# Performance work log

Hardware: AMD Instinct MI355X
Metric: run time of the kernel (lower is better)

## Reference

```python
import jax, jax.numpy as jnp
import numpy as np

EPSILON_BASE = 0.1
N_ITERS = 10


def setup_inputs() -> dict:
    key = jax.random.key(0)
    k1, k2 = jax.random.split(key)
    N, D = 8192, 512
    embeddings = jax.random.normal(k1, (N, D), dtype=jnp.float32)
    target_noise = jax.random.normal(k2, (N, D), dtype=jnp.float32)
    return {"embeddings": embeddings, "target_noise": target_noise}


def _l2_normalize(x, axis=1, eps=1e-12):
    # matches torch.nn.functional.normalize (divide by max(norm, eps))
    norm = jnp.sqrt(jnp.sum(x * x, axis=axis, keepdims=True))
    return x / jnp.maximum(norm, eps)


def _sinkhorn(x, y):
    n, d = x.shape
    # normalize_embeddings=True path
    x = _l2_normalize(x, axis=1)
    y = _l2_normalize(y, axis=1)
    epsilon = EPSILON_BASE * 2.0
    # squared euclidean cost: C[i,j] = ||x_i - y_j||^2  (cdist p=2, squared)
    sq_x = jnp.sum(x * x, axis=1, keepdims=True)          # (n,1)
    sq_y = jnp.sum(y * y, axis=1, keepdims=True)          # (n,1)
    C = jnp.maximum(sq_x + sq_y.T - 2.0 * (x @ y.T), 0.0)  # (n,n)
    log_K = -C / epsilon

    def body(carry, _):
        log_u, log_v = carry
        log_u = -jax.nn.logsumexp(log_K + log_v[None, :], axis=1)
        log_v = -jax.nn.logsumexp(log_K.T + log_u[None, :], axis=1)
        return (log_u, log_v), None

    init = (jnp.zeros(n, dtype=x.dtype), jnp.zeros(n, dtype=y.dtype))
    (log_u, log_v), _ = jax.lax.scan(body, init, None, length=N_ITERS)

    log_P = log_u[:, None] + log_K + log_v[None, :]
    P = jnp.clip(jnp.exp(log_P), 0.0, 1.0)
    distance = jnp.sum(P * C) / n

    # nan/inf fallback: 1 - mean cosine similarity (x, y already unit norm)
    fallback = 1.0 - jnp.mean(jnp.sum(x * y, axis=1))
    bad = jnp.isnan(distance) | jnp.isinf(distance)
    return jnp.where(bad, fallback, distance)


def reference(embeddings, target_noise):
    if embeddings.ndim == 3:
        embeddings = embeddings.reshape(-1, embeddings.shape[-1])
        target_noise = target_noise.reshape(-1, target_noise.shape[-1])
    return _sinkhorn(embeddings, target_noise)
```

## Files before the change

kernel.cpp:

```cpp
#include <hip/hip_runtime.h>
#include <hip/hip_bf16.h>
#include <hip/hip_fp16.h>
#include <stdint.h>

#define NROW 8192
#define DIM  512
#define LN2   0.6931471805599453f
#define TEN_LOG2E 14.426950408889634f

typedef __attribute__((ext_vector_type(8))) short short8;
typedef __attribute__((ext_vector_type(4))) float f32x4;
typedef __attribute__((ext_vector_type(2))) float f32x2;

__device__ __forceinline__ float block_sum256(float v) {
  #pragma unroll
  for (int off = 32; off > 0; off >>= 1) v += __shfl_down(v, off, 64);
  __shared__ float sb[4];
  const int w = threadIdx.x >> 6;
  if ((threadIdx.x & 63) == 0) sb[w] = v;
  __syncthreads();
  return sb[0] + sb[1] + sb[2] + sb[3];
}

__global__ __launch_bounds__(256) void init_kernel(float* __restrict__ colrcp,
                                                   float* __restrict__ diagacc,
                                                   float* __restrict__ distacc) {
  const int g = blockIdx.x * 256 + threadIdx.x;
  colrcp[g] = 1.0f;
  if (g == 0) { diagacc[0] = 0.f; distacc[0] = 0.f; }
}

__global__ __launch_bounds__(256) void normalize_kernel(
    const float* __restrict__ X, const float* __restrict__ Y,
    __hip_bfloat16* __restrict__ Xn, __hip_bfloat16* __restrict__ Yn,
    float* __restrict__ diagacc) {
  const int wave = threadIdx.x >> 6, lane = threadIdx.x & 63;
  float dsum = 0.f;
  #pragma unroll
  for (int rr = 0; rr < 4; rr++) {
    const int row = blockIdx.x * 16 + wave * 4 + rr;
    const float4* xr = (const float4*)(X + (size_t)row * DIM);
    const float4* yr = (const float4*)(Y + (size_t)row * DIM);
    float4 x0 = xr[lane], x1 = xr[lane + 64];
    float4 y0 = yr[lane], y1 = yr[lane + 64];
    float sx = x0.x*x0.x + x0.y*x0.y + x0.z*x0.z + x0.w*x0.w
             + x1.x*x1.x + x1.y*x1.y + x1.z*x1.z + x1.w*x1.w;
    float sy = y0.x*y0.x + y0.y*y0.y + y0.z*y0.z + y0.w*y0.w
             + y1.x*y1.x + y1.y*y1.y + y1.z*y1.z + y1.w*y1.w;
    float sxy = x0.x*y0.x + x0.y*y0.y + x0.z*y0.z + x0.w*y0.w
              + x1.x*y1.x + x1.y*y1.y + x1.z*y1.z + x1.w*y1.w;
    #pragma unroll
    for (int off = 1; off < 64; off <<= 1) {
      sx  += __shfl_xor(sx, off, 64);
      sy  += __shfl_xor(sy, off, 64);
      sxy += __shfl_xor(sxy, off, 64);
    }
    const float rx = 1.0f / fmaxf(sqrtf(sx), 1e-12f);
    const float ry = 1.0f / fmaxf(sqrtf(sy), 1e-12f);
    if (lane == 0) dsum += sxy * rx * ry;
    ushort4 px, py;
    { __hip_bfloat16 b;
      b = __float2bfloat16(x0.x*rx); px.x = *(unsigned short*)&b;
      b = __float2bfloat16(x0.y*rx); px.y = *(unsigned short*)&b;
      b = __float2bfloat16(x0.z*rx); px.z = *(unsigned short*)&b;
      b = __float2bfloat16(x0.w*rx); px.w = *(unsigned short*)&b;
      b = __float2bfloat16(y0.x*ry); py.x = *(unsigned short*)&b;
      b = __float2bfloat16(y0.y*ry); py.y = *(unsigned short*)&b;
      b = __float2bfloat16(y0.z*ry); py.z = *(unsigned short*)&b;
      b = __float2bfloat16(y0.w*ry); py.w = *(unsigned short*)&b;
    }
    ((ushort4*)(Xn + (size_t)row * DIM))[lane] = px;
    ((ushort4*)(Yn + (size_t)row * DIM))[lane] = py;
    { __hip_bfloat16 b;
      b = __float2bfloat16(x1.x*rx); px.x = *(unsigned short*)&b;
      b = __float2bfloat16(x1.y*rx); px.y = *(unsigned short*)&b;
      b = __float2bfloat16(x1.z*rx); px.z = *(unsigned short*)&b;
      b = __float2bfloat16(x1.w*rx); px.w = *(unsigned short*)&b;
      b = __float2bfloat16(y1.x*ry); py.x = *(unsigned short*)&b;
      b = __float2bfloat16(y1.y*ry); py.y = *(unsigned short*)&b;
      b = __float2bfloat16(y1.z*ry); py.z = *(unsigned short*)&b;
      b = __float2bfloat16(y1.w*ry); py.w = *(unsigned short*)&b;
    }
    ((ushort4*)(Xn + (size_t)row * DIM))[lane + 64] = px;
    ((ushort4*)(Yn + (size_t)row * DIM))[lane + 64] = py;
  }
  if (lane == 0) atomicAdd(diagacc, dsum);
}

__global__ __launch_bounds__(256) void gemm_kernel(
    const __hip_bfloat16* __restrict__ A, const __hip_bfloat16* __restrict__ B,
    uint8_t* __restrict__ K, uint8_t* __restrict__ KT) {
  __shared__ short As[128 * 32];
  __shared__ short Bs[128 * 32];
  const int m0 = blockIdx.y * 128;
  const int n0 = blockIdx.x * 128;
  const int t = threadIdx.x;
  const int wave = t >> 6, lane = t & 63;
  const int wm = (wave & 1) * 64, wn = (wave >> 1) * 64;
  const int fr = lane & 15;
  const int fq = lane >> 4;

  f32x4 acc[4][4];
  #pragma unroll
  for (int i = 0; i < 4; i++)
    #pragma unroll
    for (int j = 0; j < 4; j++) acc[i][j] = (f32x4)0.f;

  const int L0 = t, L1 = t + 256;
  const int ar0 = L0 >> 2, ac0 = L0 & 3;
  const int ar1 = L1 >> 2, ac1 = L1 & 3;
  const int4* Ag = (const int4*)A;
  const int4* Bg = (const int4*)B;

  for (int kt = 0; kt < 16; ++kt) {
    const int kb = kt * 4;
    int4 a0 = Ag[(size_t)(m0 + ar0) * 64 + kb + ac0];
    int4 a1 = Ag[(size_t)(m0 + ar1) * 64 + kb + ac1];
    int4 b0 = Bg[(size_t)(n0 + ar0) * 64 + kb + ac0];
    int4 b1 = Bg[(size_t)(n0 + ar1) * 64 + kb + ac1];
    __syncthreads();
    ((int4*)As)[L0] = a0;
    ((int4*)As)[L1] = a1;
    ((int4*)Bs)[L0] = b0;
    ((int4*)Bs)[L1] = b1;
    __syncthreads();
    short8 af[4], bfr[4];
    #pragma unroll
    for (int i = 0; i < 4; i++) {
      af[i]  = *(const short8*)&As[(wm + i * 16 + fr) * 32 + fq * 8];
      bfr[i] = *(const short8*)&Bs[(wn + i * 16 + fr) * 32 + fq * 8];
    }
    #pragma unroll
    for (int i = 0; i < 4; i++)
      #pragma unroll
      for (int j = 0; j < 4; j++)
        acc[i][j] = __builtin_amdgcn_mfma_f32_16x16x32_bf16(af[i], bfr[j], acc[i][j], 0, 0, 0);
  }
  #pragma unroll
  for (int i = 0; i < 4; i++) {
    #pragma unroll
    for (int j = 0; j < 4; j++) {
      const int R  = wm + i * 16 + fq * 4;
      const int Cc = wn + j * 16 + fr;
      float v0 = exp2f(fminf(acc[i][j][0], 1.0f) * TEN_LOG2E);
      float v1 = exp2f(fminf(acc[i][j][1], 1.0f) * TEN_LOG2E);
      float v2 = exp2f(fminf(acc[i][j][2], 1.0f) * TEN_LOG2E);
      float v3 = exp2f(fminf(acc[i][j][3], 1.0f) * TEN_LOG2E);
      int pk = 0;
      pk = __builtin_amdgcn_cvt_pk_fp8_f32(v0, v1, pk, false);
      pk = __builtin_amdgcn_cvt_pk_fp8_f32(v2, v3, pk, true);
      *(int*)(KT + (size_t)(n0 + Cc) * NROW + m0 + R) = pk;
      uint8_t* kp = K + (size_t)(m0 + R) * NROW + n0 + Cc;
      kp[0]            = (uint8_t)(pk & 0xff);
      kp[NROW]         = (uint8_t)((pk >> 8) & 0xff);
      kp[2 * NROW]     = (uint8_t)((pk >> 16) & 0xff);
      kp[3 * NROW]     = (uint8_t)((pk >> 24) & 0xff);
    }
  }
}

__global__ __launch_bounds__(256) void pass_kernel(
    const uint8_t* __restrict__ M, const float* __restrict__ w,
    float* __restrict__ out) {
  __shared__ float4 wl[2048];
  const int t = threadIdx.x;
  #pragma unroll
  for (int c = 0; c < 8; c++) wl[c * 256 + t] = ((const float4*)w)[c * 256 + t];
  __syncthreads();
  const int wave = t >> 6, lane = t & 63;
  const int row = blockIdx.x * 4 + wave;
  const int4* Mr = (const int4*)(M + (size_t)row * NROW);
  int4 k[8];
  #pragma unroll
  for (int c = 0; c < 8; c++) k[c] = Mr[c * 64 + lane];
  float acc0 = 0.f, acc1 = 0.f;
  #pragma unroll
  for (int c = 0; c < 8; c++) {
    const int base = (c * 64 + lane) * 4;
    const int* kd = (const int*)&k[c];
    #pragma unroll
    for (int q = 0; q < 4; q++) {
      float4 ww = wl[base + q];
      f32x2 lo = __builtin_amdgcn_cvt_pk_f32_fp8(kd[q], false);
      f32x2 hi = __builtin_amdgcn_cvt_pk_f32_fp8(kd[q], true);
      acc0 += lo.x * ww.x + lo.y * ww.y;
      acc1 += hi.x * ww.z + hi.y * ww.w;
    }
  }
  float acc = acc0 + acc1;
  #pragma unroll
  for (int off = 32; off > 0; off >>= 1) acc += __shfl_down(acc, off, 64);
  if (lane == 0) out[row] = 1.0f / acc;
}

__global__ __launch_bounds__(256) void dist_kernel(
    const uint8_t* __restrict__ K, const float* __restrict__ v,
    const float* __restrict__ u, float* __restrict__ distacc) {
  __shared__ float4 wl[2048];
  const int t = threadIdx.x;
  #pragma unroll
  for (int c = 0; c < 8; c++) wl[c * 256 + t] = ((const float4*)v)[c * 256 + t];
  __syncthreads();
  const int wave = t >> 6, lane = t & 63;
  const int row = blockIdx.x * 4 + wave;
  const float ui = u[row];
  const int4* Kr = (const int4*)(K + (size_t)row * NROW);
  float acc = 0.f;
  #pragma unroll 2
  for (int c = 0; c < 8; c++) {
    int4 kq = Kr[c * 64 + lane];
    const int base = (c * 64 + lane) * 4;
    const int* kd = (const int*)&kq;
    #pragma unroll
    for (int q = 0; q < 4; q++) {
      float4 ww = wl[base + q];
      f32x2 lo = __builtin_amdgcn_cvt_pk_f32_fp8(kd[q], false);
      f32x2 hi = __builtin_amdgcn_cvt_pk_f32_fp8(kd[q], true);
      float kv[4] = {lo.x, lo.y, hi.x, hi.y};
      float wv[4] = {ww.x, ww.y, ww.z, ww.w};
      #pragma unroll
      for (int e = 0; e < 4; e++) {
        float p = fminf(ui * kv[e] * wv[e], 1.f);
        float cterm = 2.f - 0.2f * LN2 * __log2f(fmaxf(kv[e], 1e-6f));
        acc += p * cterm;
      }
    }
  }
  float tot = block_sum256(acc);
  if (t == 0) atomicAdd(distacc, tot);
}

__global__ void final_kernel(const float* __restrict__ distacc,
                             const float* __restrict__ diagacc,
                             float* __restrict__ out) {
  if (threadIdx.x == 0 && blockIdx.x == 0) {
    float d = distacc[0] * (1.0f / (float)NROW);
    float fb = 1.0f - diagacc[0] * (1.0f / (float)NROW);
    float v = (isnan(d) || isinf(d)) ? fb : d;
    __hip_bfloat16 b = __float2bfloat16(v);
    unsigned short h = *(unsigned short*)&b;
    ((unsigned int*)out)[0] = ((unsigned int)h << 16) | (unsigned int)h;
  }
}

extern "C" void kernel_launch(void* const* d_in, const int* in_sizes, int n_in,
                              void* d_out, int out_size, void* d_ws, size_t ws_size,
                              hipStream_t stream) {
  (void)in_sizes; (void)n_in; (void)out_size; (void)ws_size;
  const float* X = (const float*)d_in[0];
  const float* Y = (const float*)d_in[1];
  float* out = (float*)d_out;

  char* ws = (char*)d_ws;
  size_t off = 0;
  uint8_t* K  = (uint8_t*)(ws + off); off += (size_t)NROW * NROW;
  uint8_t* KT = (uint8_t*)(ws + off); off += (size_t)NROW * NROW;
  __hip_bfloat16* Xn = (__hip_bfloat16*)(ws + off); off += (size_t)NROW * DIM * 2;
  __hip_bfloat16* Yn = (__hip_bfloat16*)(ws + off); off += (size_t)NROW * DIM * 2;
  float* rowrcp  = (float*)(ws + off); off += NROW * 4;
  float* colrcp  = (float*)(ws + off); off += NROW * 4;
  float* diagacc = (float*)(ws + off); off += 256;
  float* distacc = (float*)(ws + off); off += 256;

  init_kernel<<<32, 256, 0, stream>>>(colrcp, diagacc, distacc);
  normalize_kernel<<<512, 256, 0, stream>>>(X, Y, Xn, Yn, diagacc);
  gemm_kernel<<<dim3(64, 64), 256, 0, stream>>>(Xn, Yn, K, KT);
  for (int it = 0; it < 10; ++it) {
    pass_kernel<<<2048, 256, 0, stream>>>(K,  colrcp, rowrcp);
    pass_kernel<<<2048, 256, 0, stream>>>(KT, rowrcp, colrcp);
  }
  dist_kernel<<<2048, 256, 0, stream>>>(K, colrcp, rowrcp, distacc);
  final_kernel<<<1, 64, 0, stream>>>(distacc, diagacc, out);
}
```

Measured before the change: 500.2 us.

## Fuse row and column Sinkhorn passes over a single K and drop KT

Removes the transposed KT matrix. Each Sinkhorn iteration now makes one pass over K: every block of 32 rows computes the row scalings u for those rows, then accumulates that block's contribution to the column sums into a partials buffer, which a small reduce kernel turns into v. The GEMM epilogue transposes each tile through padded shared memory so K is written with coalesced 16-byte row stores instead of byte scatters, and the GEMM LDS tiles are padded to reduce bank conflicts. The aim is to halve K traffic per iteration and cut write cost in the GEMM. In exchange, each iteration adds an 8 MB partials write and read, and only 256 blocks of 512 threads are launched per pass, which may limit memory parallelism.

```diff
diff --git a/kernel.cpp b/kernel.cpp
--- a/kernel.cpp
+++ b/kernel.cpp
@@ -1,6 +1,5 @@
 #include <hip/hip_runtime.h>
 #include <hip/hip_bf16.h>
-#include <hip/hip_fp16.h>
 #include <stdint.h>
 
 #define NROW 8192
@@ -12,21 +11,11 @@
 typedef __attribute__((ext_vector_type(4))) float f32x4;
 typedef __attribute__((ext_vector_type(2))) float f32x2;
 
-__device__ __forceinline__ float block_sum256(float v) {
-  #pragma unroll
-  for (int off = 32; off > 0; off >>= 1) v += __shfl_down(v, off, 64);
-  __shared__ float sb[4];
-  const int w = threadIdx.x >> 6;
-  if ((threadIdx.x & 63) == 0) sb[w] = v;
-  __syncthreads();
-  return sb[0] + sb[1] + sb[2] + sb[3];
-}
-
-__global__ __launch_bounds__(256) void init_kernel(float* __restrict__ colrcp,
+__global__ __launch_bounds__(256) void init_kernel(float* __restrict__ v,
                                                    float* __restrict__ diagacc,
                                                    float* __restrict__ distacc) {
   const int g = blockIdx.x * 256 + threadIdx.x;
-  colrcp[g] = 1.0f;
+  v[g] = 1.0f;
   if (g == 0) { diagacc[0] = 0.f; distacc[0] = 0.f; }
 }
 
@@ -89,9 +78,12 @@
 
 __global__ __launch_bounds__(256) void gemm_kernel(
     const __hip_bfloat16* __restrict__ A, const __hip_bfloat16* __restrict__ B,
-    uint8_t* __restrict__ K, uint8_t* __restrict__ KT) {
-  __shared__ short As[128 * 32];
-  __shared__ short Bs[128 * 32];
+    uint8_t* __restrict__ K) {
+  __shared__ __align__(16) char smem[20480];
+  short* As = (short*)smem;
+  short* Bs = (short*)(smem + 10240);
+  int* tileT = (int*)smem;
+
   const int m0 = blockIdx.y * 128;
   const int n0 = blockIdx.x * 128;
   const int t = threadIdx.x;
@@ -119,16 +111,16 @@
     int4 b0 = Bg[(size_t)(n0 + ar0) * 64 + kb + ac0];
     int4 b1 = Bg[(size_t)(n0 + ar1) * 64 + kb + ac1];
     __syncthreads();
-    ((int4*)As)[L0] = a0;
-    ((int4*)As)[L1] = a1;
-    ((int4*)Bs)[L0] = b0;
-    ((int4*)Bs)[L1] = b1;
+    ((int4*)As)[ar0 * 5 + ac0] = a0;
+    ((int4*)As)[ar1 * 5 + ac1] = a1;
+    ((int4*)Bs)[ar0 * 5 + ac0] = b0;
+    ((int4*)Bs)[ar1 * 5 + ac1] = b1;
     __syncthreads();
     short8 af[4], bfr[4];
     #pragma unroll
     for (int i = 0; i < 4; i++) {
-      af[i]  = *(const short8*)&As[(wm + i * 16 + fr) * 32 + fq * 8];
-      bfr[i] = *(const short8*)&Bs[(wn + i * 16 + fr) * 32 + fq * 8];
+      af[i]  = *(const short8*)&As[(wm + i * 16 + fr) * 40 + fq * 8];
+      bfr[i] = *(const short8*)&Bs[(wn + i * 16 + fr) * 40 + fq * 8];
     }
     #pragma unroll
     for (int i = 0; i < 4; i++)
@@ -136,11 +128,12 @@
       for (int j = 0; j < 4; j++)
         acc[i][j] = __builtin_amdgcn_mfma_f32_16x16x32_bf16(af[i], bfr[j], acc[i][j], 0, 0, 0);
   }
+  __syncthreads();
   #pragma unroll
   for (int i = 0; i < 4; i++) {
     #pragma unroll
     for (int j = 0; j < 4; j++) {
-      const int R  = wm + i * 16 + fq * 4;
+      const int Rq = (wm >> 2) + i * 4 + fq;
       const int Cc = wn + j * 16 + fr;
       float v0 = exp2f(fminf(acc[i][j][0], 1.0f) * TEN_LOG2E);
       float v1 = exp2f(fminf(acc[i][j][1], 1.0f) * TEN_LOG2E);
@@ -149,85 +142,165 @@
       int pk = 0;
       pk = __builtin_amdgcn_cvt_pk_fp8_f32(v0, v1, pk, false);
       pk = __builtin_amdgcn_cvt_pk_fp8_f32(v2, v3, pk, true);
-      *(int*)(KT + (size_t)(n0 + Cc) * NROW + m0 + R) = pk;
-      uint8_t* kp = K + (size_t)(m0 + R) * NROW + n0 + Cc;
-      kp[0]            = (uint8_t)(pk & 0xff);
-      kp[NROW]         = (uint8_t)((pk >> 8) & 0xff);
-      kp[2 * NROW]     = (uint8_t)((pk >> 16) & 0xff);
-      kp[3 * NROW]     = (uint8_t)((pk >> 24) & 0xff);
-    }
-  }
-}
-
-__global__ __launch_bounds__(256) void pass_kernel(
-    const uint8_t* __restrict__ M, const float* __restrict__ w,
-    float* __restrict__ out) {
-  __shared__ float4 wl[2048];
+      tileT[Cc * 33 + Rq] = pk;
+    }
+  }
+  __syncthreads();
+  const int rl = t >> 1;
+  const int half = t & 1;
+  const int rq = rl >> 2;
+  const int rb = (rl & 3) * 8;
+  uint8_t* Krow = K + (size_t)(m0 + rl) * NROW + n0 + half * 64;
+  #pragma unroll
+  for (int q = 0; q < 4; q++) {
+    int out[4];
+    #pragma unroll
+    for (int d = 0; d < 4; d++) {
+      const int c0 = (half * 16 + q * 4 + d) * 4;
+      const unsigned w0 = (unsigned)tileT[(c0 + 0) * 33 + rq];
+      const unsigned w1 = (unsigned)tileT[(c0 + 1) * 33 + rq];
+      const unsigned w2 = (unsigned)tileT[(c0 + 2) * 33 + rq];
+      const unsigned w3 = (unsigned)tileT[(c0 + 3) * 33 + rq];
+      out[d] = (int)(((w0 >> rb) & 0xffu) | (((w1 >> rb) & 0xffu) << 8)
+                   | (((w2 >> rb) & 0xffu) << 16) | (((w3 >> rb) & 0xffu) << 24));
+    }
+    int4 o; o.x = out[0]; o.y = out[1]; o.z = out[2]; o.w = out[3];
+    ((int4*)Krow)[q] = o;
+  }
+}
+
+__global__ __launch_bounds__(512) void fused_pass_kernel(
+    const uint8_t* __restrict__ K, const float* __restrict__ v,
+    float* __restrict__ u, float* __restrict__ partials) {
+  __shared__ float wsum[8][8];
+  __shared__ float ubc[8];
   const int t = threadIdx.x;
-  #pragma unroll
-  for (int c = 0; c < 8; c++) wl[c * 256 + t] = ((const float4*)w)[c * 256 + t];
-  __syncthreads();
   const int wave = t >> 6, lane = t & 63;
-  const int row = blockIdx.x * 4 + wave;
-  const int4* Mr = (const int4*)(M + (size_t)row * NROW);
-  int4 k[8];
-  #pragma unroll
-  for (int c = 0; c < 8; c++) k[c] = Mr[c * 64 + lane];
-  float acc0 = 0.f, acc1 = 0.f;
-  #pragma unroll
-  for (int c = 0; c < 8; c++) {
-    const int base = (c * 64 + lane) * 4;
-    const int* kd = (const int*)&k[c];
-    #pragma unroll
-    for (int q = 0; q < 4; q++) {
-      float4 ww = wl[base + q];
-      f32x2 lo = __builtin_amdgcn_cvt_pk_f32_fp8(kd[q], false);
-      f32x2 hi = __builtin_amdgcn_cvt_pk_f32_fp8(kd[q], true);
-      acc0 += lo.x * ww.x + lo.y * ww.y;
-      acc1 += hi.x * ww.z + hi.y * ww.w;
-    }
-  }
-  float acc = acc0 + acc1;
-  #pragma unroll
-  for (int off = 32; off > 0; off >>= 1) acc += __shfl_down(acc, off, 64);
-  if (lane == 0) out[row] = 1.0f / acc;
-}
-
-__global__ __launch_bounds__(256) void dist_kernel(
+  const int i0 = blockIdx.x * 32;
+
+  float wv[16];
+  {
+    const float4* vp = (const float4*)(v + t * 16);
+    ((float4*)wv)[0] = vp[0]; ((float4*)wv)[1] = vp[1];
+    ((float4*)wv)[2] = vp[2]; ((float4*)wv)[3] = vp[3];
+  }
+  float acc[16];
+  #pragma unroll
+  for (int c = 0; c < 16; c++) acc[c] = 0.f;
+
+  for (int b = 0; b < 4; b++) {
+    const int rbase = i0 + b * 8;
+    int4 kd[8];
+    #pragma unroll
+    for (int r = 0; r < 8; r++)
+      kd[r] = *(const int4*)(K + (size_t)(rbase + r) * NROW + t * 16);
+    float dot[8];
+    #pragma unroll
+    for (int r = 0; r < 8; r++) {
+      const int* kp = (const int*)&kd[r];
+      float d0 = 0.f, d1 = 0.f;
+      #pragma unroll
+      for (int q = 0; q < 4; q++) {
+        f32x2 lo = __builtin_amdgcn_cvt_pk_f32_fp8(kp[q], false);
+        f32x2 hi = __builtin_amdgcn_cvt_pk_f32_fp8(kp[q], true);
+        d0 += lo.x * wv[4 * q] + lo.y * wv[4 * q + 1];
+        d1 += hi.x * wv[4 * q + 2] + hi.y * wv[4 * q + 3];
+      }
+      dot[r] = d0 + d1;
+    }
+    #pragma unroll
+    for (int r = 0; r < 8; r++)
+      #pragma unroll
+      for (int off = 1; off < 64; off <<= 1)
+        dot[r] += __shfl_xor(dot[r], off, 64);
+    if (lane == 0) {
+      #pragma unroll
+      for (int r = 0; r < 8; r++) wsum[wave][r] = dot[r];
+    }
+    __syncthreads();
+    if (t < 8) {
+      float s = wsum[0][t] + wsum[1][t] + wsum[2][t] + wsum[3][t]
+              + wsum[4][t] + wsum[5][t] + wsum[6][t] + wsum[7][t];
+      float uu = 1.0f / s;
+      ubc[t] = uu;
+      u[rbase + t] = uu;
+    }
+    __syncthreads();
+    float ur[8];
+    #pragma unroll
+    for (int r = 0; r < 8; r++) ur[r] = ubc[r];
+    #pragma unroll
+    for (int r = 0; r < 8; r++) {
+      const int* kp = (const int*)&kd[r];
+      #pragma unroll
+      for (int q = 0; q < 4; q++) {
+        f32x2 lo = __builtin_amdgcn_cvt_pk_f32_fp8(kp[q], false);
+        f32x2 hi = __builtin_amdgcn_cvt_pk_f32_fp8(kp[q], true);
+        acc[4 * q]     += lo.x * ur[r];
+        acc[4 * q + 1] += lo.y * ur[r];
+        acc[4 * q + 2] += hi.x * ur[r];
+        acc[4 * q + 3] += hi.y * ur[r];
+      }
+    }
+  }
+  float4* pp = (float4*)(partials + (size_t)blockIdx.x * NROW + t * 16);
+  pp[0] = ((float4*)acc)[0]; pp[1] = ((float4*)acc)[1];
+  pp[2] = ((float4*)acc)[2]; pp[3] = ((float4*)acc)[3];
+}
+
+__global__ __launch_bounds__(256) void vreduce_kernel(
+    const float* __restrict__ partials, float* __restrict__ v) {
+  const int j = blockIdx.x * 256 + threadIdx.x;
+  float s = 0.f;
+  #pragma unroll 8
+  for (int p = 0; p < 256; p++) s += partials[(size_t)p * NROW + j];
+  v[j] = 1.0f / s;
+}
+
+__global__ __launch_bounds__(512) void dist_kernel(
     const uint8_t* __restrict__ K, const float* __restrict__ v,
     const float* __restrict__ u, float* __restrict__ distacc) {
-  __shared__ float4 wl[2048];
+  __shared__ float uld[32];
   const int t = threadIdx.x;
-  #pragma unroll
-  for (int c = 0; c < 8; c++) wl[c * 256 + t] = ((const float4*)v)[c * 256 + t];
+  const int i0 = blockIdx.x * 32;
+  if (t < 32) uld[t] = u[i0 + t];
+  float wv[16];
+  {
+    const float4* vp = (const float4*)(v + t * 16);
+    ((float4*)wv)[0] = vp[0]; ((float4*)wv)[1] = vp[1];
+    ((float4*)wv)[2] = vp[2]; ((float4*)wv)[3] = vp[3];
+  }
   __syncthreads();
-  const int wave = t >> 6, lane = t & 63;
-  const int row = blockIdx.x * 4 + wave;
-  const float ui = u[row];
-  const int4* Kr = (const int4*)(K + (size_t)row * NROW);
   float acc = 0.f;
-  #pragma unroll 2
-  for (int c = 0; c < 8; c++) {
-    int4 kq = Kr[c * 64 + lane];
-    const int base = (c * 64 + lane) * 4;
-    const int* kd = (const int*)&kq;
+  #pragma unroll 4
+  for (int r = 0; r < 32; r++) {
+    int4 kd = *(const int4*)(K + (size_t)(i0 + r) * NROW + t * 16);
+    const float ui = uld[r];
+    const int* kp = (const int*)&kd;
     #pragma unroll
     for (int q = 0; q < 4; q++) {
-      float4 ww = wl[base + q];
-      f32x2 lo = __builtin_amdgcn_cvt_pk_f32_fp8(kd[q], false);
-      f32x2 hi = __builtin_amdgcn_cvt_pk_f32_fp8(kd[q], true);
-      float kv[4] = {lo.x, lo.y, hi.x, hi.y};
-      float wv[4] = {ww.x, ww.y, ww.z, ww.w};
+      f32x2 lo = __builtin_amdgcn_cvt_pk_f32_fp8(kp[q], false);
+      f32x2 hi = __builtin_amdgcn_cvt_pk_f32_fp8(kp[q], true);
+      float kvv[4] = {lo.x, lo.y, hi.x, hi.y};
       #pragma unroll
       for (int e = 0; e < 4; e++) {
-        float p = fminf(ui * kv[e] * wv[e], 1.f);
-        float cterm = 2.f - 0.2f * LN2 * __log2f(fmaxf(kv[e], 1e-6f));
-        acc += p * cterm;
+        float kk = kvv[e];
+        float p = fminf(ui * kk * wv[4 * q + e], 1.f);
+        float ct = 2.f - 0.2f * LN2 * __log2f(fmaxf(kk, 1e-6f));
+        acc += p * ct;
       }
     }
   }
-  float tot = block_sum256(acc);
-  if (t == 0) atomicAdd(distacc, tot);
+  #pragma unroll
+  for (int off = 32; off > 0; off >>= 1) acc += __shfl_down(acc, off, 64);
+  __shared__ float sb[8];
+  const int wave = t >> 6;
+  if ((t & 63) == 0) sb[wave] = acc;
+  __syncthreads();
+  if (t == 0) {
+    float tot = sb[0] + sb[1] + sb[2] + sb[3] + sb[4] + sb[5] + sb[6] + sb[7];
+    atomicAdd(distacc, tot);
+  }
 }
 
 __global__ void final_kernel(const float* __restrict__ distacc,
@@ -253,22 +326,22 @@
 
   char* ws = (char*)d_ws;
   size_t off = 0;
-  uint8_t* K  = (uint8_t*)(ws + off); off += (size_t)NROW * NROW;
-  uint8_t* KT = (uint8_t*)(ws + off); off += (size_t)NROW * NROW;
+  uint8_t* K = (uint8_t*)(ws + off);                off += (size_t)NROW * NROW;
+  float* partials = (float*)(ws + off);             off += (size_t)256 * NROW * 4;
   __hip_bfloat16* Xn = (__hip_bfloat16*)(ws + off); off += (size_t)NROW * DIM * 2;
   __hip_bfloat16* Yn = (__hip_bfloat16*)(ws + off); off += (size_t)NROW * DIM * 2;
-  float* rowrcp  = (float*)(ws + off); off += NROW * 4;
-  float* colrcp  = (float*)(ws + off); off += NROW * 4;
+  float* uvec = (float*)(ws + off); off += NROW * 4;
+  float* vvec = (float*)(ws + off); off += NROW * 4;
   float* diagacc = (float*)(ws + off); off += 256;
   float* distacc = (float*)(ws + off); off += 256;
 
-  init_kernel<<<32, 256, 0, stream>>>(colrcp, diagacc, distacc);
+  init_kernel<<<32, 256, 0, stream>>>(vvec, diagacc, distacc);
   normalize_kernel<<<512, 256, 0, stream>>>(X, Y, Xn, Yn, diagacc);
-  gemm_kernel<<<dim3(64, 64), 256, 0, stream>>>(Xn, Yn, K, KT);
+  gemm_kernel<<<dim3(64, 64), 256, 0, stream>>>(Xn, Yn, K);
   for (int it = 0; it < 10; ++it) {
-    pass_kernel<<<2048, 256, 0, stream>>>(K,  colrcp, rowrcp);
-    pass_kernel<<<2048, 256, 0, stream>>>(KT, rowrcp, colrcp);
-  }
-  dist_kernel<<<2048, 256, 0, stream>>>(K, colrcp, rowrcp, distacc);
+    fused_pass_kernel<<<256, 512, 0, stream>>>(K, vvec, uvec, partials);
+    vreduce_kernel<<<32, 256, 0, stream>>>(partials, vvec);
+  }
+  dist_kernel<<<256, 512, 0, stream>>>(K, vvec, uvec, distacc);
   final_kernel<<<1, 64, 0, stream>>>(distacc, diagacc, out);
 }
```

After: 539.1 us. +7.8%, slower.

## Store only transposed kernel matrix and compute row pass via column-split partials

Applied to the files above, without the earlier changes.

The GEMM now writes a single fp8 kernel matrix (transposed layout) instead of both K and KT, dropping the scattered byte stores of the second copy. The row-direction Sinkhorn pass becomes a split-reduction over 32-row slabs of the transposed matrix, writing partial sums that a separate reduce kernel combines. The column pass and the distance kernel read the same matrix. LDS tiles in the GEMM are padded to reduce bank conflicts. This halves the workspace and GEMM write traffic, at the cost of an extra partials buffer (8 MB) and an extra kernel launch per iteration.

```diff
diff --git a/kernel.cpp b/kernel.cpp
--- a/kernel.cpp
+++ b/kernel.cpp
@@ -1,6 +1,5 @@
 #include <hip/hip_runtime.h>
 #include <hip/hip_bf16.h>
-#include <hip/hip_fp16.h>
 #include <stdint.h>
 
 #define NROW 8192
@@ -12,21 +11,11 @@
 typedef __attribute__((ext_vector_type(4))) float f32x4;
 typedef __attribute__((ext_vector_type(2))) float f32x2;
 
-__device__ __forceinline__ float block_sum256(float v) {
-  #pragma unroll
-  for (int off = 32; off > 0; off >>= 1) v += __shfl_down(v, off, 64);
-  __shared__ float sb[4];
-  const int w = threadIdx.x >> 6;
-  if ((threadIdx.x & 63) == 0) sb[w] = v;
-  __syncthreads();
-  return sb[0] + sb[1] + sb[2] + sb[3];
-}
-
-__global__ __launch_bounds__(256) void init_kernel(float* __restrict__ colrcp,
+__global__ __launch_bounds__(256) void init_kernel(float* __restrict__ v,
                                                    float* __restrict__ diagacc,
                                                    float* __restrict__ distacc) {
   const int g = blockIdx.x * 256 + threadIdx.x;
-  colrcp[g] = 1.0f;
+  v[g] = 1.0f;
   if (g == 0) { diagacc[0] = 0.f; distacc[0] = 0.f; }
 }
 
@@ -89,9 +78,10 @@
 
 __global__ __launch_bounds__(256) void gemm_kernel(
     const __hip_bfloat16* __restrict__ A, const __hip_bfloat16* __restrict__ B,
-    uint8_t* __restrict__ K, uint8_t* __restrict__ KT) {
-  __shared__ short As[128 * 32];
-  __shared__ short Bs[128 * 32];
+    uint8_t* __restrict__ T) {
+  __shared__ __align__(16) short As[128 * 40];
+  __shared__ __align__(16) short Bs[128 * 40];
+
   const int m0 = blockIdx.y * 128;
   const int n0 = blockIdx.x * 128;
   const int t = threadIdx.x;
@@ -119,16 +109,16 @@
     int4 b0 = Bg[(size_t)(n0 + ar0) * 64 + kb + ac0];
     int4 b1 = Bg[(size_t)(n0 + ar1) * 64 + kb + ac1];
     __syncthreads();
-    ((int4*)As)[L0] = a0;
-    ((int4*)As)[L1] = a1;
-    ((int4*)Bs)[L0] = b0;
-    ((int4*)Bs)[L1] = b1;
+    ((int4*)As)[ar0 * 5 + ac0] = a0;
+    ((int4*)As)[ar1 * 5 + ac1] = a1;
+    ((int4*)Bs)[ar0 * 5 + ac0] = b0;
+    ((int4*)Bs)[ar1 * 5 + ac1] = b1;
     __syncthreads();
     short8 af[4], bfr[4];
     #pragma unroll
     for (int i = 0; i < 4; i++) {
-      af[i]  = *(const short8*)&As[(wm + i * 16 + fr) * 32 + fq * 8];
-      bfr[i] = *(const short8*)&Bs[(wn + i * 16 + fr) * 32 + fq * 8];
+      af[i]  = *(const short8*)&As[(wm + i * 16 + fr) * 40 + fq * 8];
+      bfr[i] = *(const short8*)&Bs[(wn + i * 16 + fr) * 40 + fq * 8];
     }
     #pragma unroll
     for (int i = 0; i < 4; i++)
@@ -137,11 +127,12 @@
         acc[i][j] = __builtin_amdgcn_mfma_f32_16x16x32_bf16(af[i], bfr[j], acc[i][j], 0, 0, 0);
   }
   #pragma unroll
-  for (int i = 0; i < 4; i++) {
-    #pragma unroll
-    for (int j = 0; j < 4; j++) {
-      const int R  = wm + i * 16 + fq * 4;
-      const int Cc = wn + j * 16 + fr;
+  for (int j = 0; j < 4; j++) {
+    const int Cc = wn + j * 16 + fr;
+    uint8_t* Trow = T + (size_t)(n0 + Cc) * NROW + m0;
+    #pragma unroll
+    for (int i = 0; i < 4; i++) {
+      const int R = wm + i * 16 + fq * 4;
       float v0 = exp2f(fminf(acc[i][j][0], 1.0f) * TEN_LOG2E);
       float v1 = exp2f(fminf(acc[i][j][1], 1.0f) * TEN_LOG2E);
       float v2 = exp2f(fminf(acc[i][j][2], 1.0f) * TEN_LOG2E);
@@ -149,85 +140,152 @@
       int pk = 0;
       pk = __builtin_amdgcn_cvt_pk_fp8_f32(v0, v1, pk, false);
       pk = __builtin_amdgcn_cvt_pk_fp8_f32(v2, v3, pk, true);
-      *(int*)(KT + (size_t)(n0 + Cc) * NROW + m0 + R) = pk;
-      uint8_t* kp = K + (size_t)(m0 + R) * NROW + n0 + Cc;
-      kp[0]            = (uint8_t)(pk & 0xff);
-      kp[NROW]         = (uint8_t)((pk >> 8) & 0xff);
-      kp[2 * NROW]     = (uint8_t)((pk >> 16) & 0xff);
-      kp[3 * NROW]     = (uint8_t)((pk >> 24) & 0xff);
-    }
-  }
-}
-
-__global__ __launch_bounds__(256) void pass_kernel(
-    const uint8_t* __restrict__ M, const float* __restrict__ w,
-    float* __restrict__ out) {
-  __shared__ float4 wl[2048];
-  const int t = threadIdx.x;
-  #pragma unroll
-  for (int c = 0; c < 8; c++) wl[c * 256 + t] = ((const float4*)w)[c * 256 + t];
+      *(int*)(Trow + R) = pk;
+    }
+  }
+}
+
+__global__ __launch_bounds__(256) void pass1_kernel(
+    const uint8_t* __restrict__ T, const float* __restrict__ v,
+    float* __restrict__ partials) {
+  __shared__ float vl[32];
+  const int t = threadIdx.x;
+  const int i0 = blockIdx.x * 2048 + t * 8;
+  const int j0 = blockIdx.y * 32;
+  if (t < 32) vl[t] = v[j0 + t];
+  __syncthreads();
+  float acc[8];
+  #pragma unroll
+  for (int e = 0; e < 8; e++) acc[e] = 0.f;
+  #pragma unroll 8
+  for (int r = 0; r < 32; r++) {
+    int2 kd = *(const int2*)(T + (size_t)(j0 + r) * NROW + i0);
+    const float w = vl[r];
+    const int* kp = (const int*)&kd;
+    f32x2 l0 = __builtin_amdgcn_cvt_pk_f32_fp8(kp[0], false);
+    f32x2 h0 = __builtin_amdgcn_cvt_pk_f32_fp8(kp[0], true);
+    f32x2 l1 = __builtin_amdgcn_cvt_pk_f32_fp8(kp[1], false);
+    f32x2 h1 = __builtin_amdgcn_cvt_pk_f32_fp8(kp[1], true);
+    acc[0] += l0.x * w; acc[1] += l0.y * w;
+    acc[2] += h0.x * w; acc[3] += h0.y * w;
+    acc[4] += l1.x * w; acc[5] += l1.y * w;
+    acc[6] += h1.x * w; acc[7] += h1.y * w;
+  }
+  float4* pp = (float4*)(partials + (size_t)blockIdx.y * NROW + i0);
+  pp[0] = ((float4*)acc)[0];
+  pp[1] = ((float4*)acc)[1];
+}
+
+__global__ __launch_bounds__(256) void ureduce_kernel(
+    const float* __restrict__ partials, float* __restrict__ u) {
+  __shared__ float red[8][32];
+  const int t = threadIdx.x;
+  const int c = t & 31, g = t >> 5;
+  const int j = blockIdx.x * 32 + c;
+  float s = 0.f;
+  #pragma unroll 8
+  for (int p = g * 32; p < g * 32 + 32; p++) s += partials[(size_t)p * NROW + j];
+  red[g][c] = s;
+  __syncthreads();
+  if (t < 32) {
+    float tot = 0.f;
+    #pragma unroll
+    for (int gg = 0; gg < 8; gg++) tot += red[gg][t];
+    u[blockIdx.x * 32 + t] = 1.0f / tot;
+  }
+}
+
+__global__ __launch_bounds__(256) void pass2_kernel(
+    const uint8_t* __restrict__ T, const float* __restrict__ u,
+    float* __restrict__ vout) {
+  __shared__ float ul[NROW];
+  const int t = threadIdx.x;
+  #pragma unroll
+  for (int c = 0; c < 8; c++)
+    ((float4*)ul)[c * 256 + t] = ((const float4*)u)[c * 256 + t];
   __syncthreads();
   const int wave = t >> 6, lane = t & 63;
-  const int row = blockIdx.x * 4 + wave;
-  const int4* Mr = (const int4*)(M + (size_t)row * NROW);
-  int4 k[8];
-  #pragma unroll
-  for (int c = 0; c < 8; c++) k[c] = Mr[c * 64 + lane];
-  float acc0 = 0.f, acc1 = 0.f;
-  #pragma unroll
-  for (int c = 0; c < 8; c++) {
-    const int base = (c * 64 + lane) * 4;
-    const int* kd = (const int*)&k[c];
-    #pragma unroll
-    for (int q = 0; q < 4; q++) {
-      float4 ww = wl[base + q];
-      f32x2 lo = __builtin_amdgcn_cvt_pk_f32_fp8(kd[q], false);
-      f32x2 hi = __builtin_amdgcn_cvt_pk_f32_fp8(kd[q], true);
-      acc0 += lo.x * ww.x + lo.y * ww.y;
-      acc1 += hi.x * ww.z + hi.y * ww.w;
-    }
-  }
-  float acc = acc0 + acc1;
+  const int rA = blockIdx.x * 8 + wave * 2;
+  const int rB = rA + 1;
+  const int2* TA = (const int2*)(T + (size_t)rA * NROW);
+  const int2* TB = (const int2*)(T + (size_t)rB * NROW);
+  const float4* ul4 = (const float4*)ul;
+  float dA = 0.f, dB = 0.f;
+  #pragma unroll 4
+  for (int c = 0; c < 16; c++) {
+    const int idx = c * 64 + lane;
+    int2 ka = TA[idx];
+    int2 kb = TB[idx];
+    float4 w0 = ul4[idx * 2];
+    float4 w1 = ul4[idx * 2 + 1];
+    const int* ap = (const int*)&ka;
+    const int* bp = (const int*)&kb;
+    {
+      f32x2 l0 = __builtin_amdgcn_cvt_pk_f32_fp8(ap[0], false);
+      f32x2 h0 = __builtin_amdgcn_cvt_pk_f32_fp8(ap[0], true);
+      f32x2 l1 = __builtin_amdgcn_cvt_pk_f32_fp8(ap[1], false);
+      f32x2 h1 = __builtin_amdgcn_cvt_pk_f32_fp8(ap[1], true);
+      dA += l0.x * w0.x + l0.y * w0.y + h0.x * w0.z + h0.y * w0.w
+          + l1.x * w1.x + l1.y * w1.y + h1.x * w1.z + h1.y * w1.w;
+    }
+    {
+      f32x2 l0 = __builtin_amdgcn_cvt_pk_f32_fp8(bp[0], false);
+      f32x2 h0 = __builtin_amdgcn_cvt_pk_f32_fp8(bp[0], true);
+      f32x2 l1 = __builtin_amdgcn_cvt_pk_f32_fp8(bp[1], false);
+      f32x2 h1 = __builtin_amdgcn_cvt_pk_f32_fp8(bp[1], true);
+      dB += l0.x * w0.x + l0.y * w0.y + h0.x * w0.z + h0.y * w0.w
+          + l1.x * w1.x + l1.y * w1.y + h1.x * w1.z + h1.y * w1.w;
+    }
+  }
+  #pragma unroll
+  for (int off = 1; off < 64; off <<= 1) {
+    dA += __shfl_xor(dA, off, 64);
+    dB += __shfl_xor(dB, off, 64);
+  }
+  if (lane == 0) {
+    vout[rA] = 1.0f / dA;
+    vout[rB] = 1.0f / dB;
+  }
+}
+
+__global__ __launch_bounds__(256) void dist_kernel(
+    const uint8_t* __restrict__ T, const float* __restrict__ u,
+    const float* __restrict__ v, float* __restrict__ distacc) {
+  __shared__ float vl[32];
+  const int t = threadIdx.x;
+  const int i0 = blockIdx.x * 2048 + t * 8;
+  const int j0 = blockIdx.y * 32;
+  if (t < 32) vl[t] = v[j0 + t];
+  float uu[8];
+  ((float4*)uu)[0] = ((const float4*)(u + i0))[0];
+  ((float4*)uu)[1] = ((const float4*)(u + i0))[1];
+  __syncthreads();
+  float acc = 0.f;
+  #pragma unroll 4
+  for (int r = 0; r < 32; r++) {
+    int2 kd = *(const int2*)(T + (size_t)(j0 + r) * NROW + i0);
+    const float w = vl[r];
+    const int* kp = (const int*)&kd;
+    f32x2 l0 = __builtin_amdgcn_cvt_pk_f32_fp8(kp[0], false);
+    f32x2 h0 = __builtin_amdgcn_cvt_pk_f32_fp8(kp[0], true);
+    f32x2 l1 = __builtin_amdgcn_cvt_pk_f32_fp8(kp[1], false);
+    f32x2 h1 = __builtin_amdgcn_cvt_pk_f32_fp8(kp[1], true);
+    float kvv[8] = {l0.x, l0.y, h0.x, h0.y, l1.x, l1.y, h1.x, h1.y};
+    #pragma unroll
+    for (int e = 0; e < 8; e++) {
+      float kk = kvv[e];
+      float p = fminf(uu[e] * kk * w, 1.f);
+      float ct = 2.f - 0.2f * LN2 * __log2f(fmaxf(kk, 1e-6f));
+      acc += p * ct;
+    }
+  }
   #pragma unroll
   for (int off = 32; off > 0; off >>= 1) acc += __shfl_down(acc, off, 64);
-  if (lane == 0) out[row] = 1.0f / acc;
-}
-
-__global__ __launch_bounds__(256) void dist_kernel(
-    const uint8_t* __restrict__ K, const float* __restrict__ v,
-    const float* __restrict__ u, float* __restrict__ distacc) {
-  __shared__ float4 wl[2048];
-  const int t = threadIdx.x;
-  #pragma unroll
-  for (int c = 0; c < 8; c++) wl[c * 256 + t] = ((const float4*)v)[c * 256 + t];
-  __syncthreads();
-  const int wave = t >> 6, lane = t & 63;
-  const int row = blockIdx.x * 4 + wave;
-  const float ui = u[row];
-  const int4* Kr = (const int4*)(K + (size_t)row * NROW);
-  float acc = 0.f;
-  #pragma unroll 2
-  for (int c = 0; c < 8; c++) {
-    int4 kq = Kr[c * 64 + lane];
-    const int base = (c * 64 + lane) * 4;
-    const int* kd = (const int*)&kq;
-    #pragma unroll
-    for (int q = 0; q < 4; q++) {
-      float4 ww = wl[base + q];
-      f32x2 lo = __builtin_amdgcn_cvt_pk_f32_fp8(kd[q], false);
-      f32x2 hi = __builtin_amdgcn_cvt_pk_f32_fp8(kd[q], true);
-      float kv[4] = {lo.x, lo.y, hi.x, hi.y};
-      float wv[4] = {ww.x, ww.y, ww.z, ww.w};
-      #pragma unroll
-      for (int e = 0; e < 4; e++) {
-        float p = fminf(ui * kv[e] * wv[e], 1.f);
-        float cterm = 2.f - 0.2f * LN2 * __log2f(fmaxf(kv[e], 1e-6f));
-        acc += p * cterm;
-      }
-    }
-  }
-  float tot = block_sum256(acc);
-  if (t == 0) atomicAdd(distacc, tot);
+  __shared__ float sb[4];
+  const int wave = t >> 6;
+  if ((t & 63) == 0) sb[wave] = acc;
+  __syncthreads();
+  if (t == 0) atomicAdd(distacc, sb[0] + sb[1] + sb[2] + sb[3]);
 }
 
 __global__ void final_kernel(const float* __restrict__ distacc,
@@ -253,22 +311,23 @@
 
   char* ws = (char*)d_ws;
   size_t off = 0;
-  uint8_t* K  = (uint8_t*)(ws + off); off += (size_t)NROW * NROW;
-  uint8_t* KT = (uint8_t*)(ws + off); off += (size_t)NROW * NROW;
+  uint8_t* T = (uint8_t*)(ws + off);                off += (size_t)NROW * NROW;
+  float* partials = (float*)(ws + off);             off += (size_t)256 * NROW * 4;
   __hip_bfloat16* Xn = (__hip_bfloat16*)(ws + off); off += (size_t)NROW * DIM * 2;
   __hip_bfloat16* Yn = (__hip_bfloat16*)(ws + off); off += (size_t)NROW * DIM * 2;
-  float* rowrcp  = (float*)(ws + off); off += NROW * 4;
-  float* colrcp  = (float*)(ws + off); off += NROW * 4;
+  float* uvec = (float*)(ws + off); off += NROW * 4;
+  float* vvec = (float*)(ws + off); off += NROW * 4;
   float* diagacc = (float*)(ws + off); off += 256;
   float* distacc = (float*)(ws + off); off += 256;
 
-  init_kernel<<<32, 256, 0, stream>>>(colrcp, diagacc, distacc);
+  init_kernel<<<32, 256, 0, stream>>>(vvec, diagacc, distacc);
   normalize_kernel<<<512, 256, 0, stream>>>(X, Y, Xn, Yn, diagacc);
-  gemm_kernel<<<dim3(64, 64), 256, 0, stream>>>(Xn, Yn, K, KT);
+  gemm_kernel<<<dim3(64, 64), 256, 0, stream>>>(Xn, Yn, T);
   for (int it = 0; it < 10; ++it) {
-    pass_kernel<<<2048, 256, 0, stream>>>(K,  colrcp, rowrcp);
-    pass_kernel<<<2048, 256, 0, stream>>>(KT, rowrcp, colrcp);
-  }
-  dist_kernel<<<2048, 256, 0, stream>>>(K, colrcp, rowrcp, distacc);
+    pass1_kernel<<<dim3(4, 256), 256, 0, stream>>>(T, vvec, partials);
+    ureduce_kernel<<<256, 256, 0, stream>>>(partials, uvec);
+    pass2_kernel<<<1024, 256, 0, stream>>>(T, uvec, vvec);
+  }
+  dist_kernel<<<dim3(4, 256), 256, 0, stream>>>(T, uvec, vvec, distacc);
   final_kernel<<<1, 64, 0, stream>>>(distacc, diagacc, out);
 }
```

After: 558.3 us. 1.12x slower.
